# Kernel tuning notes

Hardware: AMD Instinct MI355X
Metric: run time of the kernel (lower is better)

The kernel has to match this reference:

```python
import jax, jax.numpy as jnp
import numpy as np

EPS = 1e-5  # torch InstanceNorm2d default eps


def setup_inputs() -> dict:
    key = jax.random.key(0)
    ks = jax.random.split(key, 5)
    B, C, H, W = 4, 64, 64, 64
    x = jax.random.normal(ks[0], (B, C, H, W), dtype=jnp.float32)
    # Conv2d 1x1 weights as [out_c, in_c] matrices (kernel dims squeezed)
    w_qkv = jax.random.normal(ks[1], (3 * C, C), dtype=jnp.float32) * (C ** -0.5)
    b_qkv = jax.random.normal(ks[2], (3 * C,), dtype=jnp.float32) * 0.02
    w_proj = jax.random.normal(ks[3], (C, C), dtype=jnp.float32) * (C ** -0.5)
    b_proj = jax.random.normal(ks[4], (C,), dtype=jnp.float32) * 0.02
    return {"x": x, "w_qkv": w_qkv, "b_qkv": b_qkv, "w_proj": w_proj, "b_proj": b_proj}


def reference(x, w_qkv, b_qkv, w_proj, b_proj):
    B, C, H, W = x.shape
    scale = C ** -0.5
    # InstanceNorm2d(affine=False): per-(B,C) stats over spatial dims, biased var
    mean = jnp.mean(x, axis=(2, 3), keepdims=True)
    var = jnp.var(x, axis=(2, 3), keepdims=True)
    h = (x - mean) * jax.lax.rsqrt(var + EPS)
    # 1x1 conv qkv projection: [B,3C,H,W]
    qkv = jnp.einsum('bchw,oc->bohw', h, w_qkv) + b_qkv[None, :, None, None]
    q, k, v = jnp.split(qkv, 3, axis=1)
    HW = H * W
    q = q.reshape(B, C, HW).transpose(0, 2, 1)  # [B, HW, C]
    k = k.reshape(B, C, HW)                      # [B, C, HW]
    v = v.reshape(B, C, HW).transpose(0, 2, 1)  # [B, HW, C]
    attn = jnp.einsum('bnc,bcm->bnm', q, k) * scale  # [B, HW, HW]
    attn = jax.nn.softmax(attn, axis=-1)
    # dropout p=0.0 -> identity
    h = jnp.einsum('bnm,bmc->bnc', attn, v)          # [B, HW, C]
    h = h.transpose(0, 2, 1).reshape(B, C, H, W)
    h = jnp.einsum('bchw,oc->bohw', h, w_proj) + b_proj[None, :, None, None]
    return x + h
```

## Files before the change

kernel.cpp:

```cpp
#include <hip/hip_runtime.h>
#include <hip/hip_bf16.h>

#define B_ 4
#define C_ 64
#define N_ 4096
#define EPS_ 1e-5f
#define C2_ 0.18033688011112042f

typedef __hip_bfloat16 bf16;
typedef __attribute__((ext_vector_type(8))) short short8;
typedef __attribute__((ext_vector_type(4))) float f32x4;

__device__ __forceinline__ float b2f(bf16 v) { return __bfloat162float(v); }

__device__ __forceinline__ short f2bs(float f) {
  union { bf16 h; short s; } u;
  u.h = __float2bfloat16(f);
  return u.s;
}

__device__ __forceinline__ short8 pk8(const float* f) {
  union { short8 v; short s[8]; } u;
#pragma unroll
  for (int i = 0; i < 8; ++i) u.s[i] = f2bs(f[i]);
  return u.v;
}

__device__ __forceinline__ void up8(short8 v, float* d) {
  union { short8 v; unsigned u[4]; } x;
  x.v = v;
  d[0] = __uint_as_float(x.u[0] << 16);
  d[1] = __uint_as_float(x.u[0] & 0xffff0000u);
  d[2] = __uint_as_float(x.u[1] << 16);
  d[3] = __uint_as_float(x.u[1] & 0xffff0000u);
  d[4] = __uint_as_float(x.u[2] << 16);
  d[5] = __uint_as_float(x.u[2] & 0xffff0000u);
  d[6] = __uint_as_float(x.u[3] << 16);
  d[7] = __uint_as_float(x.u[3] & 0xffff0000u);
}

template <bool F32>
__device__ __forceinline__ float ldx(const void* p, size_t idx) {
  if (F32) return ((const float*)p)[idx];
  return b2f(((const bf16*)p)[idx]);
}


__device__ __forceinline__ size_t q_off(int b, int n, int c) {
  const int strip = n >> 4, ks = c >> 5, qd = (c >> 3) & 3, jj = c & 7, li = n & 15;
  return ((((size_t)(b * 256 + strip)) * 2 + ks) * 64 + qd * 16 + li) * 8 + jj;
}
__device__ __forceinline__ size_t k_off(int b, int n, int c) {
  const int kt = n >> 6, nb = (n >> 4) & 3, ks = c >> 5;
  const int qd = (c >> 3) & 3, jj = c & 7, li = n & 15;
  return ((((size_t)(b * 64 + kt)) * 8 + nb * 2 + ks) * 64 + qd * 16 + li) * 8 + jj;
}
__device__ __forceinline__ size_t v_off(int b, int n, int c) {
  const int jt = n >> 6, nb = c >> 4, ks = (n >> 5) & 1;
  const int qd = (n >> 3) & 3, jj = n & 7, li = c & 15;
  return ((((size_t)(b * 64 + jt)) * 8 + nb * 2 + ks) * 64 + qd * 16 + li) * 8 + jj;
}

__device__ __forceinline__ void cwrite(short* pb, int rb, int cb, int r,
                                       int quad, int li, float v) {
  const int frag = rb * 2 + (cb >> 1);
  const int kloc = (cb & 1) * 16 + li;
  const int l2 = (kloc >> 3) * 16 + quad * 4 + r;
  pb[frag * 512 + ((l2 ^ (l2 >> 3)) << 3) + (kloc & 7)] = f2bs(v);
}
__device__ __forceinline__ short8 cread(const short* pb, int frag, int l) {
  return *(const short8*)&pb[frag * 512 + ((l ^ (l >> 3)) << 3)];
}

__global__ __launch_bounds__(256) void k_detect(const ushort* __restrict__ xr,
                                                int* __restrict__ flag) {
  const int t = threadIdx.x;
  int cnt = 0;
  for (int i = t; i < 8192; i += 256) {
    const int e = (xr[i] >> 7) & 0xFF;
    if (e >= 143) ++cnt;
  }
#pragma unroll
  for (int off = 32; off > 0; off >>= 1) cnt += __shfl_down(cnt, off, 64);
  __shared__ int pc[4];
  if ((t & 63) == 0) pc[t >> 6] = cnt;
  __syncthreads();
  if (t == 0) flag[0] = (pc[0] + pc[1] + pc[2] + pc[3] > 64) ? 1 : 0;
}

template <bool F32>
__device__ __forceinline__ void stats_body(const void* x, float* meanArr,
                                           float* rstdArr) {
  const int bc = blockIdx.x;
  const size_t base = (size_t)bc * N_;
  const int t = threadIdx.x;
  float s = 0.f, s2 = 0.f;
#pragma unroll
  for (int r = 0; r < N_ / 256; ++r) {
    const float v = ldx<F32>(x, base + t + 256 * r);
    s += v;
    s2 += v * v;
  }
#pragma unroll
  for (int off = 32; off > 0; off >>= 1) {
    s += __shfl_down(s, off, 64);
    s2 += __shfl_down(s2, off, 64);
  }
  __shared__ float ps[4], ps2[4];
  if ((t & 63) == 0) { ps[t >> 6] = s; ps2[t >> 6] = s2; }
  __syncthreads();
  if (t == 0) {
    const float S = ps[0] + ps[1] + ps[2] + ps[3];
    const float S2 = ps2[0] + ps2[1] + ps2[2] + ps2[3];
    const float mean = S * (1.0f / N_);
    const float var = S2 * (1.0f / N_) - mean * mean;
    meanArr[bc] = mean;
    rstdArr[bc] = rsqrtf(var + EPS_);
  }
}
__global__ __launch_bounds__(256) void k_stats(const void* __restrict__ x,
                                               float* __restrict__ meanArr,
                                               float* __restrict__ rstdArr,
                                               const int* __restrict__ flag) {
  if (*flag) stats_body<true>(x, meanArr, rstdArr);
  else stats_body<false>(x, meanArr, rstdArr);
}

template <bool F32>
__device__ __forceinline__ void qkv_body(const void* x, const void* wqkv,
                                         const void* bqkv, const float* meanArr,
                                         const float* rstdArr, bf16* q, bf16* k,
                                         bf16* v, short* HB) {
  const int t = threadIdx.x;
  const int tj = blockIdx.x;
  const int b = blockIdx.y;
  const int n0 = tj * 64;
  {
    const int li = t & 15, nbt = (t >> 4) & 3, cg = t >> 6;
    const int n = n0 + nbt * 16 + li;
    const float* mb_ = meanArr + b * 64;
    const float* rb_ = rstdArr + b * 64;
    float hv[16];
#pragma unroll
    for (int i = 0; i < 16; ++i) {
      const int c = cg * 16 + i;
      const float xv = ldx<F32>(x, ((size_t)(b * 64 + c)) * N_ + n);
      hv[i] = (xv - mb_[c]) * rb_[c];
    }
#pragma unroll
    for (int c8 = 0; c8 < 2; ++c8) {
      const int ks = cg >> 1, qd = (cg & 1) * 2 + c8;
      *(short8*)&HB[((nbt * 2 + ks) * 64 + qd * 16 + li) * 8] = pk8(&hv[c8 * 8]);
    }
  }
  __syncthreads();
  const int l = t & 63, w = t >> 6, li = l & 15, quad = l >> 4;
  short8 A[3][2];
#pragma unroll
  for (int j = 0; j < 3; ++j) {
    const int o = (w * 3 + j) * 16 + li;
#pragma unroll
    for (int ks = 0; ks < 2; ++ks) {
      const int cbase = ks * 32 + quad * 8;
      if (F32) {
        float tmp[8];
#pragma unroll
        for (int i = 0; i < 8; ++i) tmp[i] = ((const float*)wqkv)[o * 64 + cbase + i];
        A[j][ks] = pk8(tmp);
      } else {
        A[j][ks] = *(const short8*)((const bf16*)wqkv + o * 64 + cbase);
      }
    }
  }
  short8 Bv[4][2];
#pragma unroll
  for (int nb = 0; nb < 4; ++nb)
#pragma unroll
    for (int ks = 0; ks < 2; ++ks)
      Bv[nb][ks] = *(const short8*)&HB[((nb * 2 + ks) * 64 + l) * 8];
  f32x4 D[3][4];
#pragma unroll
  for (int j = 0; j < 3; ++j)
#pragma unroll
    for (int nb = 0; nb < 4; ++nb) {
      f32x4 acc = {0.f, 0.f, 0.f, 0.f};
      acc = __builtin_amdgcn_mfma_f32_16x16x32_bf16(A[j][0], Bv[nb][0], acc, 0, 0, 0);
      acc = __builtin_amdgcn_mfma_f32_16x16x32_bf16(A[j][1], Bv[nb][1], acc, 0, 0, 0);
      D[j][nb] = acc;
    }
#pragma unroll
  for (int j = 0; j < 3; ++j) {
    const int ob = w * 3 + j;
    float bv[4];
#pragma unroll
    for (int r = 0; r < 4; ++r) bv[r] = ldx<F32>(bqkv, ob * 16 + quad * 4 + r);
    if (ob < 8) {
#pragma unroll
      for (int nb = 0; nb < 4; ++nb) {
        const int n = n0 + nb * 16 + li;
        union { ushort4 u4; short s[4]; } pkd;
#pragma unroll
        for (int r = 0; r < 4; ++r) pkd.s[r] = f2bs(D[j][nb][r] + bv[r]);
        const int o0 = ob * 16 + quad * 4;
        if (ob < 4) {
          *(ushort4*)&q[q_off(b, n, o0)] = pkd.u4;
        } else {
          *(ushort4*)&k[k_off(b, n, o0 - 64)] = pkd.u4;
        }
      }
    } else {
#pragma unroll
      for (int nb = 0; nb < 4; ++nb) {
        const int n = n0 + nb * 16 + li;
#pragma unroll
        for (int r = 0; r < 4; ++r)
          v[v_off(b, n, (ob - 8) * 16 + quad * 4 + r)] =
              __float2bfloat16(D[j][nb][r] + bv[r]);
      }
    }
  }
}
__global__ __launch_bounds__(256) void k_qkv(
    const void* __restrict__ x, const void* __restrict__ wqkv,
    const void* __restrict__ bqkv, const float* __restrict__ meanArr,
    const float* __restrict__ rstdArr, bf16* __restrict__ q,
    bf16* __restrict__ k, bf16* __restrict__ v, const int* __restrict__ flag) {
  __shared__ short HB[4096];
  if (*flag) qkv_body<true>(x, wqkv, bqkv, meanArr, rstdArr, q, k, v, HB);
  else qkv_body<false>(x, wqkv, bqkv, meanArr, rstdArr, q, k, v, HB);
}

template <bool F32>
__device__ __forceinline__ void attn_body(const bf16* qg, const bf16* kg,
                                          const bf16* vg, const void* xg,
                                          const void* wp, const void* bp,
                                          void* outv, short* PB,
                                          float (*lsum)[64], float* linv) {
  const int bid = blockIdx.x;
  const int b = bid & 3, qbase = (bid >> 2) * 64;
  const int t = threadIdx.x, l = t & 63, w = t >> 6, li = l & 15, quad = l >> 4;
  short* pb = PB + w * 4096;

  short8 Qf[4][2];
#pragma unroll
  for (int mb = 0; mb < 4; ++mb)
#pragma unroll
    for (int ks = 0; ks < 2; ++ks)
      Qf[mb][ks] = *(const short8*)(qg +
          ((size_t)((b * 256 + (qbase >> 4) + mb) * 2 + ks)) * 512 + l * 8);

  f32x4 O[4][4];
#pragma unroll
  for (int mb = 0; mb < 4; ++mb)
#pragma unroll
    for (int cb = 0; cb < 4; ++cb) O[mb][cb] = {0.f, 0.f, 0.f, 0.f};
  float ls[4][4] = {};

  for (int it = 0; it < 16; ++it) {
    const int kt = it * 4 + w;
    const size_t tbase = ((size_t)(b * 64 + kt)) * 8 * 512;
    short8 Kf[4][2];
#pragma unroll
    for (int nb = 0; nb < 4; ++nb)
#pragma unroll
      for (int ks = 0; ks < 2; ++ks)
        Kf[nb][ks] = *(const short8*)(kg + tbase + (nb * 2 + ks) * 512 + l * 8);
    f32x4 S[4][4];
#pragma unroll
    for (int mb = 0; mb < 4; ++mb)
#pragma unroll
      for (int nb = 0; nb < 4; ++nb) {
        f32x4 acc = {0.f, 0.f, 0.f, 0.f};
        acc = __builtin_amdgcn_mfma_f32_16x16x32_bf16(Qf[mb][0], Kf[nb][0], acc, 0, 0, 0);
        acc = __builtin_amdgcn_mfma_f32_16x16x32_bf16(Qf[mb][1], Kf[nb][1], acc, 0, 0, 0);
        S[mb][nb] = acc;
      }
    short8 Vf[4][2];
#pragma unroll
    for (int cb = 0; cb < 4; ++cb)
#pragma unroll
      for (int ks = 0; ks < 2; ++ks)
        Vf[cb][ks] = *(const short8*)(vg + tbase + (cb * 2 + ks) * 512 + l * 8);
#pragma unroll
    for (int mb = 0; mb < 4; ++mb)
#pragma unroll
      for (int nb = 0; nb < 4; ++nb)
#pragma unroll
        for (int r = 0; r < 4; ++r) {
          const float p = exp2f(S[mb][nb][r] * C2_);
          ls[mb][r] += p;
          cwrite(pb, mb, nb, r, quad, li, p);
        }
    short8 Pf[4][2];
#pragma unroll
    for (int mb = 0; mb < 4; ++mb)
#pragma unroll
      for (int ks = 0; ks < 2; ++ks) Pf[mb][ks] = cread(pb, mb * 2 + ks, l);
#pragma unroll
    for (int mb = 0; mb < 4; ++mb)
#pragma unroll
      for (int cb = 0; cb < 4; ++cb) {
        f32x4 acc = O[mb][cb];
        acc = __builtin_amdgcn_mfma_f32_16x16x32_bf16(Pf[mb][0], Vf[cb][0], acc, 0, 0, 0);
        acc = __builtin_amdgcn_mfma_f32_16x16x32_bf16(Pf[mb][1], Vf[cb][1], acc, 0, 0, 0);
        O[mb][cb] = acc;
      }
  }
#pragma unroll
  for (int mb = 0; mb < 4; ++mb)
#pragma unroll
    for (int r = 0; r < 4; ++r) {
      float v_ = ls[mb][r];
      v_ += __shfl_xor(v_, 1, 64);
      v_ += __shfl_xor(v_, 2, 64);
      v_ += __shfl_xor(v_, 4, 64);
      v_ += __shfl_xor(v_, 8, 64);
      ls[mb][r] = v_;
    }
  if (li == 0) {
#pragma unroll
    for (int mb = 0; mb < 4; ++mb)
#pragma unroll
      for (int r = 0; r < 4; ++r) lsum[w][mb * 16 + quad * 4 + r] = ls[mb][r];
  }
#pragma unroll
  for (int mb = 0; mb < 4; ++mb)
#pragma unroll
    for (int cb = 0; cb < 4; ++cb)
#pragma unroll
      for (int r = 0; r < 4; ++r) cwrite(pb, mb, cb, r, quad, li, O[mb][cb][r]);
  __syncthreads();
  if (t < 64)
    linv[t] = 1.0f / (lsum[0][t] + lsum[1][t] + lsum[2][t] + lsum[3][t]);
  __syncthreads();
  short8 Wa[2];
#pragma unroll
  for (int ks = 0; ks < 2; ++ks) {
    const int o = w * 16 + li;
    const int cbase = ks * 32 + quad * 8;
    if (F32) {
      float tmp[8];
#pragma unroll
      for (int i = 0; i < 8; ++i) tmp[i] = ((const float*)wp)[o * 64 + cbase + i];
      Wa[ks] = pk8(tmp);
    } else {
      Wa[ks] = *(const short8*)((const bf16*)wp + o * 64 + cbase);
    }
  }
  f32x4 Dp[4];
#pragma unroll
  for (int nb = 0; nb < 4; ++nb) {
    f32x4 acc = {0.f, 0.f, 0.f, 0.f};
    const float sc = linv[nb * 16 + li];
#pragma unroll
    for (int ks = 0; ks < 2; ++ks) {
      float s8[8] = {};
#pragma unroll
      for (int ww = 0; ww < 4; ++ww) {
        float tmp[8];
        up8(cread(PB + ww * 4096, nb * 2 + ks, l), tmp);
#pragma unroll
        for (int i = 0; i < 8; ++i) s8[i] += tmp[i];
      }
#pragma unroll
      for (int i = 0; i < 8; ++i) s8[i] *= sc;
      const short8 Bf = pk8(s8);
      acc = __builtin_amdgcn_mfma_f32_16x16x32_bf16(Wa[ks], Bf, acc, 0, 0, 0);
    }
    Dp[nb] = acc;
  }
  float bpv[4];
#pragma unroll
  for (int r = 0; r < 4; ++r) bpv[r] = ldx<F32>(bp, w * 16 + quad * 4 + r);
#pragma unroll
  for (int nb = 0; nb < 4; ++nb)
#pragma unroll
    for (int r = 0; r < 4; ++r) {
      const int o = w * 16 + quad * 4 + r;
      const int n = qbase + nb * 16 + li;
      const size_t idx = ((size_t)(b * 64 + o)) * N_ + n;
      const float res = ldx<F32>(xg, idx) + Dp[nb][r] + bpv[r];
      if (F32) ((float*)outv)[idx] = res;
      else ((bf16*)outv)[idx] = __float2bfloat16(res);
    }
}
__global__ __launch_bounds__(256, 1) void k_attn(
    const bf16* __restrict__ qg, const bf16* __restrict__ kg,
    const bf16* __restrict__ vg, const void* __restrict__ xg,
    const void* __restrict__ wp, const void* __restrict__ bp,
    void* __restrict__ outv, const int* __restrict__ flag) {
  __shared__ short PB[4 * 4096];
  __shared__ float lsum[4][64];
  __shared__ float linv[64];
  if (*flag) attn_body<true>(qg, kg, vg, xg, wp, bp, outv, PB, lsum, linv);
  else attn_body<false>(qg, kg, vg, xg, wp, bp, outv, PB, lsum, linv);
}

extern "C" void kernel_launch(void* const* d_in, const int* in_sizes, int n_in,
                              void* d_out, int out_size, void* d_ws,
                              size_t ws_size, hipStream_t stream) {
  const void* x = d_in[0];
  const void* wqkv = d_in[1];
  const void* bqkv = d_in[2];
  const void* wproj = d_in[3];
  const void* bproj = d_in[4];

  float* meanArr = (float*)d_ws;
  float* rstdArr = meanArr + 256;
  bf16* q = (bf16*)((char*)d_ws + 2048);
  bf16* k = q + (size_t)B_ * C_ * N_;
  bf16* v = k + (size_t)B_ * C_ * N_;
  int* flag = (int*)(v + (size_t)B_ * C_ * N_);

  k_detect<<<1, 256, 0, stream>>>((const ushort*)x, flag);
  k_stats<<<B_ * C_, 256, 0, stream>>>(x, meanArr, rstdArr, flag);
  k_qkv<<<dim3(N_ / 64, B_), 256, 0, stream>>>(x, wqkv, bqkv, meanArr, rstdArr,
                                               q, k, v, flag);
  k_attn<<<B_ * (N_ / 64), 256, 0, stream>>>(q, k, v, x, wproj, bproj, d_out,
                                             flag);
}
```

Measured before the change: 131.2 us.

## Split attention over key halves, keep P in registers, add separate projection kernel

Merges dtype detection into the stats kernel with vectorized loads, and rewrites QKV stores with a new V layout. The attention kernel now splits the key range in two (512 blocks, 2 per CU) and computes S^T so that P feeds a 16x16x16 MFMA straight from registers, removing the LDS round-trip for P. Each block writes fp32 partial O and row sums to workspace. A new projection kernel combines the two halves, normalizes, and applies the output projection and residual. This gives more parallelism and less LDS traffic, at the cost of extra global traffic for partials and one more launch.

```diff
diff --git a/kernel.cpp b/kernel.cpp
--- a/kernel.cpp
+++ b/kernel.cpp
@@ -9,6 +9,7 @@
 
 typedef __hip_bfloat16 bf16;
 typedef __attribute__((ext_vector_type(8))) short short8;
+typedef __attribute__((ext_vector_type(4))) short short4v;
 typedef __attribute__((ext_vector_type(4))) float f32x4;
 
 __device__ __forceinline__ float b2f(bf16 v) { return __bfloat162float(v); }
@@ -45,85 +46,94 @@
   return b2f(((const bf16*)p)[idx]);
 }
 
-
-__device__ __forceinline__ size_t q_off(int b, int n, int c) {
-  const int strip = n >> 4, ks = c >> 5, qd = (c >> 3) & 3, jj = c & 7, li = n & 15;
-  return ((((size_t)(b * 256 + strip)) * 2 + ks) * 64 + qd * 16 + li) * 8 + jj;
-}
-__device__ __forceinline__ size_t k_off(int b, int n, int c) {
-  const int kt = n >> 6, nb = (n >> 4) & 3, ks = c >> 5;
-  const int qd = (c >> 3) & 3, jj = c & 7, li = n & 15;
-  return ((((size_t)(b * 64 + kt)) * 8 + nb * 2 + ks) * 64 + qd * 16 + li) * 8 + jj;
-}
-__device__ __forceinline__ size_t v_off(int b, int n, int c) {
-  const int jt = n >> 6, nb = c >> 4, ks = (n >> 5) & 1;
-  const int qd = (n >> 3) & 3, jj = n & 7, li = c & 15;
-  return ((((size_t)(b * 64 + jt)) * 8 + nb * 2 + ks) * 64 + qd * 16 + li) * 8 + jj;
-}
-
-__device__ __forceinline__ void cwrite(short* pb, int rb, int cb, int r,
-                                       int quad, int li, float v) {
-  const int frag = rb * 2 + (cb >> 1);
-  const int kloc = (cb & 1) * 16 + li;
-  const int l2 = (kloc >> 3) * 16 + quad * 4 + r;
-  pb[frag * 512 + ((l2 ^ (l2 >> 3)) << 3) + (kloc & 7)] = f2bs(v);
-}
-__device__ __forceinline__ short8 cread(const short* pb, int frag, int l) {
-  return *(const short8*)&pb[frag * 512 + ((l ^ (l >> 3)) << 3)];
-}
-
-__global__ __launch_bounds__(256) void k_detect(const ushort* __restrict__ xr,
-                                                int* __restrict__ flag) {
-  const int t = threadIdx.x;
-  int cnt = 0;
-  for (int i = t; i < 8192; i += 256) {
-    const int e = (xr[i] >> 7) & 0xFF;
-    if (e >= 143) ++cnt;
-  }
-#pragma unroll
-  for (int off = 32; off > 0; off >>= 1) cnt += __shfl_down(cnt, off, 64);
-  __shared__ int pc[4];
-  if ((t & 63) == 0) pc[t >> 6] = cnt;
-  __syncthreads();
-  if (t == 0) flag[0] = (pc[0] + pc[1] + pc[2] + pc[3] > 64) ? 1 : 0;
-}
-
 template <bool F32>
-__device__ __forceinline__ void stats_body(const void* x, float* meanArr,
-                                           float* rstdArr) {
-  const int bc = blockIdx.x;
-  const size_t base = (size_t)bc * N_;
-  const int t = threadIdx.x;
+__device__ __forceinline__ short8 ld8(const void* p, int idx) {
+  if (F32) {
+    const float* fp = (const float*)p + idx;
+    float tmp[8];
+    *(float4*)&tmp[0] = *(const float4*)fp;
+    *(float4*)&tmp[4] = *(const float4*)(fp + 4);
+    return pk8(tmp);
+  }
+  return *(const short8*)((const bf16*)p + idx);
+}
+
+__device__ __forceinline__ f32x4 mfma32(short8 a, short8 b, f32x4 c) {
+  return __builtin_amdgcn_mfma_f32_16x16x32_bf16(a, b, c, 0, 0, 0);
+}
+__device__ __forceinline__ f32x4 mfma16(short4v a, short4v b, f32x4 c) {
+  return __builtin_amdgcn_mfma_f32_16x16x16bf16_1k(a, b, c, 0, 0, 0);
+}
+
+
+template <bool F32>
+__device__ __forceinline__ void stats_sum(const void* x, int bc, int t,
+                                          float& s, float& s2) {
+  if (F32) {
+    const float4* xp = (const float4*)((const float*)x + (size_t)bc * N_);
+#pragma unroll
+    for (int r = 0; r < 4; ++r) {
+      const float4 v = xp[r * 256 + t];
+      s += (v.x + v.y) + (v.z + v.w);
+      s2 += (v.x * v.x + v.y * v.y) + (v.z * v.z + v.w * v.w);
+    }
+  } else {
+    const bf16* xp = (const bf16*)x + (size_t)bc * N_;
+#pragma unroll
+    for (int r = 0; r < 2; ++r) {
+      float f[8];
+      up8(*(const short8*)(xp + (r * 256 + t) * 8), f);
+#pragma unroll
+      for (int i = 0; i < 8; ++i) { s += f[i]; s2 += f[i] * f[i]; }
+    }
+  }
+}
+
+__global__ __launch_bounds__(256) void k_stats(const void* __restrict__ x,
+                                               float* __restrict__ meanArr,
+                                               float* __restrict__ rstdArr,
+                                               int* __restrict__ flag) {
+  const int bc = blockIdx.x, t = threadIdx.x;
+  __shared__ float ps[4], ps2[4];
+  __shared__ int pflag;
+  {
+    const ushort* xw = (const ushort*)x + (size_t)bc * 4096;
+    int cnt = 0;
+#pragma unroll
+    for (int j = 0; j < 4; ++j) {
+      const ushort4 u = *(const ushort4*)(xw + t * 16 + j * 4);
+      cnt += ((u.x >> 7) & 0xFF) >= 143;
+      cnt += ((u.y >> 7) & 0xFF) >= 143;
+      cnt += ((u.z >> 7) & 0xFF) >= 143;
+      cnt += ((u.w >> 7) & 0xFF) >= 143;
+    }
+#pragma unroll
+    for (int off = 32; off > 0; off >>= 1) cnt += __shfl_down(cnt, off, 64);
+    if (t == 0) pflag = 0;
+    __syncthreads();
+    if ((t & 63) == 0 && cnt > 16) atomicAdd(&pflag, cnt);
+    __syncthreads();
+  }
+  const bool f32 = pflag > 64;
   float s = 0.f, s2 = 0.f;
-#pragma unroll
-  for (int r = 0; r < N_ / 256; ++r) {
-    const float v = ldx<F32>(x, base + t + 256 * r);
-    s += v;
-    s2 += v * v;
-  }
+  if (f32) stats_sum<true>(x, bc, t, s, s2);
+  else stats_sum<false>(x, bc, t, s, s2);
 #pragma unroll
   for (int off = 32; off > 0; off >>= 1) {
     s += __shfl_down(s, off, 64);
     s2 += __shfl_down(s2, off, 64);
   }
-  __shared__ float ps[4], ps2[4];
   if ((t & 63) == 0) { ps[t >> 6] = s; ps2[t >> 6] = s2; }
   __syncthreads();
   if (t == 0) {
-    const float S = ps[0] + ps[1] + ps[2] + ps[3];
-    const float S2 = ps2[0] + ps2[1] + ps2[2] + ps2[3];
+    const float S = (ps[0] + ps[1]) + (ps[2] + ps[3]);
+    const float S2 = (ps2[0] + ps2[1]) + (ps2[2] + ps2[3]);
     const float mean = S * (1.0f / N_);
     const float var = S2 * (1.0f / N_) - mean * mean;
     meanArr[bc] = mean;
     rstdArr[bc] = rsqrtf(var + EPS_);
-  }
-}
-__global__ __launch_bounds__(256) void k_stats(const void* __restrict__ x,
-                                               float* __restrict__ meanArr,
-                                               float* __restrict__ rstdArr,
-                                               const int* __restrict__ flag) {
-  if (*flag) stats_body<true>(x, meanArr, rstdArr);
-  else stats_body<false>(x, meanArr, rstdArr);
+    flag[0] = f32 ? 1 : 0;
+  }
 }
 
 template <bool F32>
@@ -131,9 +141,7 @@
                                          const void* bqkv, const float* meanArr,
                                          const float* rstdArr, bf16* q, bf16* k,
                                          bf16* v, short* HB) {
-  const int t = threadIdx.x;
-  const int tj = blockIdx.x;
-  const int b = blockIdx.y;
+  const int t = threadIdx.x, tj = blockIdx.x, b = blockIdx.y;
   const int n0 = tj * 64;
   {
     const int li = t & 15, nbt = (t >> 4) & 3, cg = t >> 6;
@@ -144,8 +152,7 @@
 #pragma unroll
     for (int i = 0; i < 16; ++i) {
       const int c = cg * 16 + i;
-      const float xv = ldx<F32>(x, ((size_t)(b * 64 + c)) * N_ + n);
-      hv[i] = (xv - mb_[c]) * rb_[c];
+      hv[i] = (ldx<F32>(x, ((size_t)(b * 64 + c)) * N_ + n) - mb_[c]) * rb_[c];
     }
 #pragma unroll
     for (int c8 = 0; c8 < 2; ++c8) {
@@ -155,69 +162,46 @@
   }
   __syncthreads();
   const int l = t & 63, w = t >> 6, li = l & 15, quad = l >> 4;
-  short8 A[3][2];
-#pragma unroll
-  for (int j = 0; j < 3; ++j) {
-    const int o = (w * 3 + j) * 16 + li;
-#pragma unroll
-    for (int ks = 0; ks < 2; ++ks) {
-      const int cbase = ks * 32 + quad * 8;
-      if (F32) {
-        float tmp[8];
-#pragma unroll
-        for (int i = 0; i < 8; ++i) tmp[i] = ((const float*)wqkv)[o * 64 + cbase + i];
-        A[j][ks] = pk8(tmp);
-      } else {
-        A[j][ks] = *(const short8*)((const bf16*)wqkv + o * 64 + cbase);
-      }
-    }
-  }
-  short8 Bv[4][2];
+  short8 Wf[3][2];
+#pragma unroll
+  for (int sec = 0; sec < 3; ++sec)
+#pragma unroll
+    for (int ks = 0; ks < 2; ++ks)
+      Wf[sec][ks] = ld8<F32>(wqkv, (sec * 64 + w * 16 + li) * 64 + ks * 32 + quad * 8);
+  short8 Hf[4][2];
 #pragma unroll
   for (int nb = 0; nb < 4; ++nb)
 #pragma unroll
     for (int ks = 0; ks < 2; ++ks)
-      Bv[nb][ks] = *(const short8*)&HB[((nb * 2 + ks) * 64 + l) * 8];
-  f32x4 D[3][4];
-#pragma unroll
-  for (int j = 0; j < 3; ++j)
-#pragma unroll
-    for (int nb = 0; nb < 4; ++nb) {
-      f32x4 acc = {0.f, 0.f, 0.f, 0.f};
-      acc = __builtin_amdgcn_mfma_f32_16x16x32_bf16(A[j][0], Bv[nb][0], acc, 0, 0, 0);
-      acc = __builtin_amdgcn_mfma_f32_16x16x32_bf16(A[j][1], Bv[nb][1], acc, 0, 0, 0);
-      D[j][nb] = acc;
-    }
-#pragma unroll
-  for (int j = 0; j < 3; ++j) {
-    const int ob = w * 3 + j;
-    float bv[4];
-#pragma unroll
-    for (int r = 0; r < 4; ++r) bv[r] = ldx<F32>(bqkv, ob * 16 + quad * 4 + r);
-    if (ob < 8) {
-#pragma unroll
-      for (int nb = 0; nb < 4; ++nb) {
-        const int n = n0 + nb * 16 + li;
-        union { ushort4 u4; short s[4]; } pkd;
-#pragma unroll
-        for (int r = 0; r < 4; ++r) pkd.s[r] = f2bs(D[j][nb][r] + bv[r]);
-        const int o0 = ob * 16 + quad * 4;
-        if (ob < 4) {
-          *(ushort4*)&q[q_off(b, n, o0)] = pkd.u4;
-        } else {
-          *(ushort4*)&k[k_off(b, n, o0 - 64)] = pkd.u4;
-        }
-      }
-    } else {
-#pragma unroll
-      for (int nb = 0; nb < 4; ++nb) {
-        const int n = n0 + nb * 16 + li;
-#pragma unroll
-        for (int r = 0; r < 4; ++r)
-          v[v_off(b, n, (ob - 8) * 16 + quad * 4 + r)] =
-              __float2bfloat16(D[j][nb][r] + bv[r]);
-      }
-    }
+      Hf[nb][ks] = *(const short8*)&HB[((nb * 2 + ks) * 64 + l) * 8];
+  float bq[4], bk[4];
+#pragma unroll
+  for (int r = 0; r < 4; ++r) {
+    bq[r] = ldx<F32>(bqkv, w * 16 + quad * 4 + r);
+    bk[r] = ldx<F32>(bqkv, 64 + w * 16 + quad * 4 + r);
+  }
+  const float bv = ldx<F32>(bqkv, 128 + w * 16 + li);
+  const int lhi = ((w & 1) * 2 + (quad >> 1)) * 16 + li;
+  const int jj0 = (quad & 1) * 4;
+#pragma unroll
+  for (int nb = 0; nb < 4; ++nb) {
+    f32x4 dq = {0.f, 0.f, 0.f, 0.f}, dk = dq, dv = dq;
+    dq = mfma32(Wf[0][0], Hf[nb][0], dq);
+    dq = mfma32(Wf[0][1], Hf[nb][1], dq);
+    dk = mfma32(Wf[1][0], Hf[nb][0], dk);
+    dk = mfma32(Wf[1][1], Hf[nb][1], dk);
+    dv = mfma32(Hf[nb][0], Wf[2][0], dv);
+    dv = mfma32(Hf[nb][1], Wf[2][1], dv);
+    union { ushort4 u; short s[4]; } pq, pk_, pv;
+#pragma unroll
+    for (int r = 0; r < 4; ++r) {
+      pq.s[r] = f2bs(dq[r] + bq[r]);
+      pk_.s[r] = f2bs(dk[r] + bk[r]);
+      pv.s[r] = f2bs(dv[r] + bv);
+    }
+    *(ushort4*)&q[(((size_t)(b * 256 + tj * 4 + nb)) * 2 + (w >> 1)) * 512 + lhi * 8 + jj0] = pq.u;
+    *(ushort4*)&k[(((size_t)(b * 64 + tj)) * 8 + nb * 2 + (w >> 1)) * 512 + lhi * 8 + jj0] = pk_.u;
+    *(ushort4*)&v[(((size_t)(b * 64 + tj)) * 16 + w * 4 + nb) * 256 + (quad * 16 + li) * 4] = pv.u;
   }
 }
 __global__ __launch_bounds__(256) void k_qkv(
@@ -230,170 +214,167 @@
   else qkv_body<false>(x, wqkv, bqkv, meanArr, rstdArr, q, k, v, HB);
 }
 
+__global__ __launch_bounds__(256, 2) void k_attn(
+    const bf16* __restrict__ qg, const bf16* __restrict__ kg,
+    const bf16* __restrict__ vg, float* __restrict__ opart,
+    float* __restrict__ lpart) {
+  __shared__ float Oacc[64][68];
+  __shared__ float lsum[4][64];
+  const int bid = blockIdx.x;
+  const int b = bid & 3, qt = (bid >> 2) & 63, kh = bid >> 8;
+  const int t = threadIdx.x, l = t & 63, w = t >> 6, li = l & 15, quad = l >> 4;
+
+  short8 Qf[4][2];
+#pragma unroll
+  for (int mb = 0; mb < 4; ++mb)
+#pragma unroll
+    for (int ks = 0; ks < 2; ++ks)
+      Qf[mb][ks] = *(const short8*)(qg + (((size_t)(b * 256 + qt * 4 + mb)) * 2 + ks) * 512 + l * 8);
+
+  f32x4 O[4][4];
+#pragma unroll
+  for (int cb = 0; cb < 4; ++cb)
+#pragma unroll
+    for (int mb = 0; mb < 4; ++mb) O[cb][mb] = {0.f, 0.f, 0.f, 0.f};
+  float ls[4] = {0.f, 0.f, 0.f, 0.f};
+
+  for (int it = 0; it < 8; ++it) {
+    const int kt = kh * 32 + it * 4 + w;
+    const size_t kb = ((size_t)(b * 64 + kt)) * 8 * 512;
+    short8 Kf[4][2];
+#pragma unroll
+    for (int jb = 0; jb < 4; ++jb)
+#pragma unroll
+      for (int ks = 0; ks < 2; ++ks)
+        Kf[jb][ks] = *(const short8*)(kg + kb + (jb * 2 + ks) * 512 + l * 8);
+    const size_t vb = ((size_t)(b * 64 + kt)) * 16 * 256;
+    short4v Vf[4][4];
+#pragma unroll
+    for (int cb = 0; cb < 4; ++cb)
+#pragma unroll
+      for (int jb = 0; jb < 4; ++jb)
+        Vf[cb][jb] = *(const short4v*)(vg + vb + (cb * 4 + jb) * 256 + l * 4);
+#pragma unroll
+    for (int jb = 0; jb < 4; ++jb) {
+      short4v Pf[4];
+#pragma unroll
+      for (int mb = 0; mb < 4; ++mb) {
+        f32x4 s = {0.f, 0.f, 0.f, 0.f};
+        s = mfma32(Kf[jb][0], Qf[mb][0], s);
+        s = mfma32(Kf[jb][1], Qf[mb][1], s);
+        const float p0 = exp2f(s[0] * C2_), p1 = exp2f(s[1] * C2_);
+        const float p2 = exp2f(s[2] * C2_), p3 = exp2f(s[3] * C2_);
+        ls[mb] += (p0 + p1) + (p2 + p3);
+        union { short4v v; __hip_bfloat162 h[2]; } pu;
+        pu.h[0] = __float22bfloat162_rn(make_float2(p0, p1));
+        pu.h[1] = __float22bfloat162_rn(make_float2(p2, p3));
+        Pf[mb] = pu.v;
+      }
+#pragma unroll
+      for (int cb = 0; cb < 4; ++cb)
+#pragma unroll
+        for (int mb = 0; mb < 4; ++mb)
+          O[cb][mb] = mfma16(Vf[cb][jb], Pf[mb], O[cb][mb]);
+    }
+  }
+#pragma unroll
+  for (int mb = 0; mb < 4; ++mb) {
+    ls[mb] += __shfl_xor(ls[mb], 16, 64);
+    ls[mb] += __shfl_xor(ls[mb], 32, 64);
+  }
+  if (l < 16) {
+#pragma unroll
+    for (int mb = 0; mb < 4; ++mb) lsum[w][mb * 16 + l] = ls[mb];
+  }
+  for (int ph = 0; ph < 4; ++ph) {
+    if (w == ph) {
+#pragma unroll
+      for (int cb = 0; cb < 4; ++cb)
+#pragma unroll
+        for (int mb = 0; mb < 4; ++mb) {
+          float4* dst = (float4*)&Oacc[mb * 16 + li][cb * 16 + quad * 4];
+          float4 val;
+          val.x = O[cb][mb][0]; val.y = O[cb][mb][1];
+          val.z = O[cb][mb][2]; val.w = O[cb][mb][3];
+          if (ph == 0) *dst = val;
+          else {
+            float4 cur = *dst;
+            cur.x += val.x; cur.y += val.y; cur.z += val.z; cur.w += val.w;
+            *dst = cur;
+          }
+        }
+    }
+    __syncthreads();
+  }
+  if (t < 64)
+    lpart[(((size_t)(kh * 4 + b)) * 64 + qt) * 64 + t] =
+        ((lsum[0][t] + lsum[1][t]) + (lsum[2][t] + lsum[3][t]));
+  const size_t obase = (((size_t)(kh * 4 + b)) * 64 + qt) * 4096;
+  const int m = t >> 2, cs = (t & 3) * 16;
+#pragma unroll
+  for (int k4 = 0; k4 < 4; ++k4)
+    *(float4*)&opart[obase + m * 64 + cs + k4 * 4] =
+        *(const float4*)&Oacc[m][cs + k4 * 4];
+}
+
 template <bool F32>
-__device__ __forceinline__ void attn_body(const bf16* qg, const bf16* kg,
-                                          const bf16* vg, const void* xg,
-                                          const void* wp, const void* bp,
-                                          void* outv, short* PB,
-                                          float (*lsum)[64], float* linv) {
-  const int bid = blockIdx.x;
-  const int b = bid & 3, qbase = (bid >> 2) * 64;
+__device__ __forceinline__ void proj_body(const float* opart, const float* lpart,
+                                          const void* xg, const void* wp,
+                                          const void* bp, void* outv) {
+  const int qt = blockIdx.x, b = blockIdx.y;
   const int t = threadIdx.x, l = t & 63, w = t >> 6, li = l & 15, quad = l >> 4;
-  short* pb = PB + w * 4096;
-
-  short8 Qf[4][2];
+  short8 Wa[2];
+#pragma unroll
+  for (int ks = 0; ks < 2; ++ks)
+    Wa[ks] = ld8<F32>(wp, (w * 16 + li) * 64 + ks * 32 + quad * 8);
+  const size_t ob0 = (((size_t)b) * 64 + qt) * 4096;
+  const size_t ob1 = (((size_t)(4 + b)) * 64 + qt) * 4096;
+  const size_t lb0 = (((size_t)b) * 64 + qt) * 64;
+  const size_t lb1 = (((size_t)(4 + b)) * 64 + qt) * 64;
+  float bpv[4];
+#pragma unroll
+  for (int r = 0; r < 4; ++r) bpv[r] = ldx<F32>(bp, w * 16 + quad * 4 + r);
+  f32x4 D[4];
+#pragma unroll
+  for (int mb = 0; mb < 4; ++mb) {
+    const int m = mb * 16 + li;
+    const float lv = 1.0f / (lpart[lb0 + m] + lpart[lb1 + m]);
+    f32x4 acc = {0.f, 0.f, 0.f, 0.f};
+#pragma unroll
+    for (int ks = 0; ks < 2; ++ks) {
+      const int cb0 = ks * 32 + quad * 8;
+      float s8[8];
+      *(float4*)&s8[0] = *(const float4*)&opart[ob0 + m * 64 + cb0];
+      *(float4*)&s8[4] = *(const float4*)&opart[ob0 + m * 64 + cb0 + 4];
+      const float4 t1 = *(const float4*)&opart[ob1 + m * 64 + cb0];
+      const float4 t2 = *(const float4*)&opart[ob1 + m * 64 + cb0 + 4];
+      s8[0] += t1.x; s8[1] += t1.y; s8[2] += t1.z; s8[3] += t1.w;
+      s8[4] += t2.x; s8[5] += t2.y; s8[6] += t2.z; s8[7] += t2.w;
+#pragma unroll
+      for (int i = 0; i < 8; ++i) s8[i] *= lv;
+      acc = mfma32(Wa[ks], pk8(s8), acc);
+    }
+    D[mb] = acc;
+  }
 #pragma unroll
   for (int mb = 0; mb < 4; ++mb)
-#pragma unroll
-    for (int ks = 0; ks < 2; ++ks)
-      Qf[mb][ks] = *(const short8*)(qg +
-          ((size_t)((b * 256 + (qbase >> 4) + mb) * 2 + ks)) * 512 + l * 8);
-
-  f32x4 O[4][4];
-#pragma unroll
-  for (int mb = 0; mb < 4; ++mb)
-#pragma unroll
-    for (int cb = 0; cb < 4; ++cb) O[mb][cb] = {0.f, 0.f, 0.f, 0.f};
-  float ls[4][4] = {};
-
-  for (int it = 0; it < 16; ++it) {
-    const int kt = it * 4 + w;
-    const size_t tbase = ((size_t)(b * 64 + kt)) * 8 * 512;
-    short8 Kf[4][2];
-#pragma unroll
-    for (int nb = 0; nb < 4; ++nb)
-#pragma unroll
-      for (int ks = 0; ks < 2; ++ks)
-        Kf[nb][ks] = *(const short8*)(kg + tbase + (nb * 2 + ks) * 512 + l * 8);
-    f32x4 S[4][4];
-#pragma unroll
-    for (int mb = 0; mb < 4; ++mb)
-#pragma unroll
-      for (int nb = 0; nb < 4; ++nb) {
-        f32x4 acc = {0.f, 0.f, 0.f, 0.f};
-        acc = __builtin_amdgcn_mfma_f32_16x16x32_bf16(Qf[mb][0], Kf[nb][0], acc, 0, 0, 0);
-        acc = __builtin_amdgcn_mfma_f32_16x16x32_bf16(Qf[mb][1], Kf[nb][1], acc, 0, 0, 0);
-        S[mb][nb] = acc;
-      }
-    short8 Vf[4][2];
-#pragma unroll
-    for (int cb = 0; cb < 4; ++cb)
-#pragma unroll
-      for (int ks = 0; ks < 2; ++ks)
-        Vf[cb][ks] = *(const short8*)(vg + tbase + (cb * 2 + ks) * 512 + l * 8);
-#pragma unroll
-    for (int mb = 0; mb < 4; ++mb)
-#pragma unroll
-      for (int nb = 0; nb < 4; ++nb)
-#pragma unroll
-        for (int r = 0; r < 4; ++r) {
-          const float p = exp2f(S[mb][nb][r] * C2_);
-          ls[mb][r] += p;
-          cwrite(pb, mb, nb, r, quad, li, p);
-        }
-    short8 Pf[4][2];
-#pragma unroll
-    for (int mb = 0; mb < 4; ++mb)
-#pragma unroll
-      for (int ks = 0; ks < 2; ++ks) Pf[mb][ks] = cread(pb, mb * 2 + ks, l);
-#pragma unroll
-    for (int mb = 0; mb < 4; ++mb)
-#pragma unroll
-      for (int cb = 0; cb < 4; ++cb) {
-        f32x4 acc = O[mb][cb];
-        acc = __builtin_amdgcn_mfma_f32_16x16x32_bf16(Pf[mb][0], Vf[cb][0], acc, 0, 0, 0);
-        acc = __builtin_amdgcn_mfma_f32_16x16x32_bf16(Pf[mb][1], Vf[cb][1], acc, 0, 0, 0);
-        O[mb][cb] = acc;
-      }
-  }
-#pragma unroll
-  for (int mb = 0; mb < 4; ++mb)
-#pragma unroll
-    for (int r = 0; r < 4; ++r) {
-      float v_ = ls[mb][r];
-      v_ += __shfl_xor(v_, 1, 64);
-      v_ += __shfl_xor(v_, 2, 64);
-      v_ += __shfl_xor(v_, 4, 64);
-      v_ += __shfl_xor(v_, 8, 64);
-      ls[mb][r] = v_;
-    }
-  if (li == 0) {
-#pragma unroll
-    for (int mb = 0; mb < 4; ++mb)
-#pragma unroll
-      for (int r = 0; r < 4; ++r) lsum[w][mb * 16 + quad * 4 + r] = ls[mb][r];
-  }
-#pragma unroll
-  for (int mb = 0; mb < 4; ++mb)
-#pragma unroll
-    for (int cb = 0; cb < 4; ++cb)
-#pragma unroll
-      for (int r = 0; r < 4; ++r) cwrite(pb, mb, cb, r, quad, li, O[mb][cb][r]);
-  __syncthreads();
-  if (t < 64)
-    linv[t] = 1.0f / (lsum[0][t] + lsum[1][t] + lsum[2][t] + lsum[3][t]);
-  __syncthreads();
-  short8 Wa[2];
-#pragma unroll
-  for (int ks = 0; ks < 2; ++ks) {
-    const int o = w * 16 + li;
-    const int cbase = ks * 32 + quad * 8;
-    if (F32) {
-      float tmp[8];
-#pragma unroll
-      for (int i = 0; i < 8; ++i) tmp[i] = ((const float*)wp)[o * 64 + cbase + i];
-      Wa[ks] = pk8(tmp);
-    } else {
-      Wa[ks] = *(const short8*)((const bf16*)wp + o * 64 + cbase);
-    }
-  }
-  f32x4 Dp[4];
-#pragma unroll
-  for (int nb = 0; nb < 4; ++nb) {
-    f32x4 acc = {0.f, 0.f, 0.f, 0.f};
-    const float sc = linv[nb * 16 + li];
-#pragma unroll
-    for (int ks = 0; ks < 2; ++ks) {
-      float s8[8] = {};
-#pragma unroll
-      for (int ww = 0; ww < 4; ++ww) {
-        float tmp[8];
-        up8(cread(PB + ww * 4096, nb * 2 + ks, l), tmp);
-#pragma unroll
-        for (int i = 0; i < 8; ++i) s8[i] += tmp[i];
-      }
-#pragma unroll
-      for (int i = 0; i < 8; ++i) s8[i] *= sc;
-      const short8 Bf = pk8(s8);
-      acc = __builtin_amdgcn_mfma_f32_16x16x32_bf16(Wa[ks], Bf, acc, 0, 0, 0);
-    }
-    Dp[nb] = acc;
-  }
-  float bpv[4];
-#pragma unroll
-  for (int r = 0; r < 4; ++r) bpv[r] = ldx<F32>(bp, w * 16 + quad * 4 + r);
-#pragma unroll
-  for (int nb = 0; nb < 4; ++nb)
 #pragma unroll
     for (int r = 0; r < 4; ++r) {
       const int o = w * 16 + quad * 4 + r;
-      const int n = qbase + nb * 16 + li;
+      const int n = qt * 64 + mb * 16 + li;
       const size_t idx = ((size_t)(b * 64 + o)) * N_ + n;
-      const float res = ldx<F32>(xg, idx) + Dp[nb][r] + bpv[r];
+      const float res = ldx<F32>(xg, idx) + D[mb][r] + bpv[r];
       if (F32) ((float*)outv)[idx] = res;
       else ((bf16*)outv)[idx] = __float2bfloat16(res);
     }
 }
-__global__ __launch_bounds__(256, 1) void k_attn(
-    const bf16* __restrict__ qg, const bf16* __restrict__ kg,
-    const bf16* __restrict__ vg, const void* __restrict__ xg,
-    const void* __restrict__ wp, const void* __restrict__ bp,
-    void* __restrict__ outv, const int* __restrict__ flag) {
-  __shared__ short PB[4 * 4096];
-  __shared__ float lsum[4][64];
-  __shared__ float linv[64];
-  if (*flag) attn_body<true>(qg, kg, vg, xg, wp, bp, outv, PB, lsum, linv);
-  else attn_body<false>(qg, kg, vg, xg, wp, bp, outv, PB, lsum, linv);
+__global__ __launch_bounds__(256) void k_proj(
+    const float* __restrict__ opart, const float* __restrict__ lpart,
+    const void* __restrict__ xg, const void* __restrict__ wp,
+    const void* __restrict__ bp, void* __restrict__ outv,
+    const int* __restrict__ flag) {
+  if (*flag) proj_body<true>(opart, lpart, xg, wp, bp, outv);
+  else proj_body<false>(opart, lpart, xg, wp, bp, outv);
 }
 
 extern "C" void kernel_launch(void* const* d_in, const int* in_sizes, int n_in,
@@ -405,17 +386,20 @@
   const void* wproj = d_in[3];
   const void* bproj = d_in[4];
 
-  float* meanArr = (float*)d_ws;
-  float* rstdArr = meanArr + 256;
-  bf16* q = (bf16*)((char*)d_ws + 2048);
-  bf16* k = q + (size_t)B_ * C_ * N_;
-  bf16* v = k + (size_t)B_ * C_ * N_;
-  int* flag = (int*)(v + (size_t)B_ * C_ * N_);
-
-  k_detect<<<1, 256, 0, stream>>>((const ushort*)x, flag);
-  k_stats<<<B_ * C_, 256, 0, stream>>>(x, meanArr, rstdArr, flag);
-  k_qkv<<<dim3(N_ / 64, B_), 256, 0, stream>>>(x, wqkv, bqkv, meanArr, rstdArr,
-                                               q, k, v, flag);
-  k_attn<<<B_ * (N_ / 64), 256, 0, stream>>>(q, k, v, x, wproj, bproj, d_out,
-                                             flag);
-}
+  char* ws = (char*)d_ws;
+  float* meanArr = (float*)ws;
+  float* rstdArr = (float*)(ws + 1024);
+  int* flag = (int*)(ws + 2048);
+  bf16* q = (bf16*)(ws + 4096);
+  bf16* k = (bf16*)(ws + 4096 + (2u << 20));
+  bf16* v = (bf16*)(ws + 4096 + (4u << 20));
+  float* opart = (float*)(ws + 4096 + (6u << 20));
+  float* lpart = (float*)(ws + 4096 + (14u << 20));
+
+  k_stats<<<256, 256, 0, stream>>>(x, meanArr, rstdArr, flag);
+  k_qkv<<<dim3(64, 4), 256, 0, stream>>>(x, wqkv, bqkv, meanArr, rstdArr, q, k,
+                                         v, flag);
+  k_attn<<<512, 256, 0, stream>>>(q, k, v, opart, lpart);
+  k_proj<<<dim3(64, 4), 256, 0, stream>>>(opart, lpart, x, wproj, bproj, d_out,
+                                          flag);
+}
```

New measurement: 120.9 us. 7.8% less time.
